# Performance work log

Measured on AMD Instinct MI355X. Metric: run time of the kernel, lower is better.

Reference implementation:

```python
import jax, jax.numpy as jnp
import numpy as np
from jax import lax


def _f(x, t, params):
    # Neural-ODE vector field: MLP acting on last dim (t unused, as allowed by arbitrary f)
    W1, b1, W2 = params
    return jnp.tanh(x @ W1 + b1) @ W2


def _euler_step(f, x, t, dt, params):
    return x + dt * f(x, t, params)


def _rk4_step(f, x, t, dt, params):
    # Replicates the source tableau EXACTLY, including its c-index offsets
    # (k2 uses t + c[0]*dt = t, k3 uses t + c[1]*dt, k4 uses t + c[2]*dt).
    c = (0.0, 0.5, 0.5, 1.0)
    k1 = f(x, t, params)
    k2 = f(x + dt * (0.5 * k1), t + c[0] * dt, params)
    k3 = f(x + dt * (0.5 * k2), t + c[1] * dt, params)
    k4 = f(x + dt * k3, t + c[2] * dt, params)
    return x + dt * (k1 / 6.0 + k2 / 3.0 + k3 / 3.0 + k4 / 6.0)


def _integrate(step, f, x, ts, params):
    # fixed_odeint with t = ts[k], dt = ts[k+1]-ts[k]; returns final state only
    dts = ts[1:] - ts[:-1]
    def body(xc, tdt):
        t, dt = tdt
        return step(f, xc, t, dt, params), None
    xf, _ = lax.scan(body, x, (ts[:-1], dts))
    return xf


def setup_inputs() -> dict:
    key = jax.random.key(0)
    k1, k2, k3 = jax.random.split(key, 3)
    n_sub, batch, d, h = 16, 256, 1024, 4096
    B = jax.random.normal(k1, (n_sub, batch, d), jnp.float32)
    t_span = jnp.arange(n_sub, dtype=jnp.float32)
    W1 = jax.random.normal(k2, (d, h), jnp.float32) * 0.02
    b1 = jnp.zeros((h,), jnp.float32)
    W2 = jax.random.normal(k3, (h, d), jnp.float32) * 0.02
    return {"B": B, "t_span": t_span, "W1": W1, "b1": b1, "W2": W2,
            "fine_steps": 8, "maxiter": 2}


def reference(B, t_span, W1, b1, W2, fine_steps, maxiter):
    params = (W1, b1, W2)
    n = B.shape[0]                       # n_subinterv
    dt = t_span[1] - t_span[0]
    sub_ts = jnp.linspace(0.0, dt, fine_steps)
    # Original: i = 0; while i <= maxiter: i += 1; body(i)  ->  i = 1..maxiter+1
    for i in range(1, maxiter + 2):
        # coarse (Euler) and fine (RK4) sweeps over all remaining nodes, vectorized
        B_coarse = _integrate(_euler_step, _f, B[i - 1:], sub_ts, params)  # [n-i+1,b,d]
        B_fine = _integrate(_rk4_step, _f, B[i - 1:], sub_ts, params)
        # sequential Parareal correction over nodes m = i..n-1
        def inner(B_in, cf):
            Bc, Bf = cf
            nxt = _integrate(_euler_step, _f, B_in, sub_ts, params) - Bc + Bf
            return nxt, nxt
        _, tail = lax.scan(inner, B[i - 1], (B_coarse[: n - i], B_fine[: n - i]))
        B = jnp.concatenate([B[:i], tail], axis=0)
    return B
```

## Files before the change

kernel.cpp:

```cpp
#include <hip/hip_runtime.h>
#include <cstdint>
#include <cstddef>


typedef __attribute__((ext_vector_type(4))) float f32x4;
typedef __attribute__((ext_vector_type(8))) short s16x8;
typedef __attribute__((ext_vector_type(4))) unsigned short u16x4;

#define DEV __device__ __forceinline__

DEV unsigned short f2bf(float x) {
  union { float f; uint32_t u; } v; v.f = x;
  uint32_t r = v.u + 0x7FFFu + ((v.u >> 16) & 1u);
  return (unsigned short)(r >> 16);
}
DEV float bf2f(unsigned short h) {
  union { uint32_t u; float f; } v; v.u = ((uint32_t)h) << 16; return v.f;
}
DEV void split2(float x, unsigned short &h, unsigned short &l) {
  h = f2bf(x);
  l = f2bf(x - bf2f(h));
}
DEV float fast_tanh(float z) {
  return 1.f - 2.f / (__expf(2.f * z) + 1.f);
}
DEV void gload16(const unsigned short* g, unsigned short* l) {
  __builtin_amdgcn_global_load_lds(
      (const __attribute__((address_space(1))) void*)g,
      (__attribute__((address_space(3))) void*)l, 16, 0, 0);
}

template<int EPI>
__global__ __launch_bounds__(256, 2) void gemm_k(
    const unsigned short* __restrict__ Ah, const unsigned short* __restrict__ Al,
    const unsigned short* __restrict__ Bh, const unsigned short* __restrict__ Bl,
    const float* __restrict__ bias,
    unsigned short* __restrict__ Oh, unsigned short* __restrict__ Ol,
    const float* __restrict__ Xin,
    float* __restrict__ ACCb,
    float* __restrict__ Xout,
    const float* __restrict__ tspan,
    float a1, float a2, int accAdd,
    int M, int N, int K, int KS)
{
  __shared__ unsigned short sA[2][128 * 64];
  __shared__ unsigned short sB[2][128 * 64];
  const int tid = threadIdx.x;
  const int w = tid >> 6, l = tid & 63;
  const int m0 = blockIdx.y * 128, n0 = blockIdx.x * 128;
  const int wm = (w >> 1) * 64, wn = (w & 1) * 64;

  f32x4 acc[4][4];
#pragma unroll
  for (int a = 0; a < 4; ++a)
#pragma unroll
    for (int b = 0; b < 4; ++b) acc[a][b] = (f32x4){0.f, 0.f, 0.f, 0.f};

  const int rsub = w * 8 + (l >> 3);
  const int ssrc = (l & 7) ^ (l >> 3);
  const int shalf = ssrc >> 2;
  const int schunk = ssrc & 3;
  const unsigned short* gA = (shalf ? Al : Ah) + (size_t)(m0 + rsub) * K + schunk * 8;
  const unsigned short* gB = (shalf ? Bl : Bh) + (size_t)(n0 + rsub) * K + schunk * 8;
  const size_t gstep = (size_t)32 * (size_t)K;
  const int db = w * 512;

  const int arow = (l & 15);
  const int slotH = ((l >> 4)) ^ (l & 7);
  const int slotL = (4 + (l >> 4)) ^ (l & 7);

  const int nk = KS >> 5;

  auto STAGE = [&](int buf, int kt) {
    const size_t ko = (size_t)kt * 32;
    unsigned short* da = &sA[buf][db];
    unsigned short* dbp = &sB[buf][db];
#pragma unroll
    for (int j = 0; j < 4; ++j) {
      gload16(gA + ko + (size_t)j * gstep, da + j * 2048);
      gload16(gB + ko + (size_t)j * gstep, dbp + j * 2048);
    }
  };

  STAGE(0, 0);
  __syncthreads();
  int cur = 0;

  for (int kt = 0; kt < nk; ++kt) {
    if (kt + 1 < nk) STAGE(cur ^ 1, kt + 1);
    const unsigned short* pa = &sA[cur][0];
    const unsigned short* pb = &sB[cur][0];
    s16x8 afh[4], afl[4], bfh[4], bfl[4];
#pragma unroll
    for (int mi = 0; mi < 4; ++mi) {
      const int rb = (wm + mi * 16 + arow) * 64;
      afh[mi] = *(const s16x8*)&pa[rb + slotH * 8];
      afl[mi] = *(const s16x8*)&pa[rb + slotL * 8];
    }
#pragma unroll
    for (int ni = 0; ni < 4; ++ni) {
      const int rb = (wn + ni * 16 + arow) * 64;
      bfh[ni] = *(const s16x8*)&pb[rb + slotH * 8];
      bfl[ni] = *(const s16x8*)&pb[rb + slotL * 8];
    }
#pragma unroll
    for (int mi = 0; mi < 4; ++mi)
#pragma unroll
      for (int ni = 0; ni < 4; ++ni) {
        acc[mi][ni] = __builtin_amdgcn_mfma_f32_16x16x32_bf16(afh[mi], bfh[ni], acc[mi][ni], 0, 0, 0);
        acc[mi][ni] = __builtin_amdgcn_mfma_f32_16x16x32_bf16(afh[mi], bfl[ni], acc[mi][ni], 0, 0, 0);
        acc[mi][ni] = __builtin_amdgcn_mfma_f32_16x16x32_bf16(afl[mi], bfh[ni], acc[mi][ni], 0, 0, 0);
      }
    __syncthreads();
    cur ^= 1;
  }

  const int colb = n0 + wn + (l & 15);
  const int rowb = m0 + wm + (l >> 4) * 4;
  const float sdt = (EPI >= 3) ? (tspan[1] - tspan[0]) * (1.0f / 7.0f) : 0.f;

  if (EPI == 1) {
#pragma unroll
    for (int mi = 0; mi < 4; ++mi)
#pragma unroll
      for (int ni = 0; ni < 4; ++ni) {
        const int col = colb + ni * 16;
        const float bc = bias[col];
#pragma unroll
        for (int j = 0; j < 4; ++j) {
          const size_t idx = (size_t)(rowb + mi * 16 + j) * N + col;
          const float v = fast_tanh(acc[mi][ni][j] + bc);
          unsigned short hh, ll; split2(v, hh, ll);
          Oh[idx] = hh; Ol[idx] = ll;
        }
      }
  } else if (EPI == 3) {
    const float c1 = a1 * sdt, c2 = a2 * sdt;
#pragma unroll
    for (int mi = 0; mi < 4; ++mi)
#pragma unroll
      for (int ni = 0; ni < 4; ++ni) {
        const int col = colb + ni * 16;
#pragma unroll
        for (int j = 0; j < 4; ++j) {
          const size_t idx = (size_t)(rowb + mi * 16 + j) * N + col;
          const float f = acc[mi][ni][j];
          const float x = Xin[idx];
          const float a = (accAdd ? ACCb[idx] : x) + c1 * f;
          ACCb[idx] = a;
          const float xt = x + c2 * f;
          unsigned short hh, ll; split2(xt, hh, ll);
          Oh[idx] = hh; Ol[idx] = ll;
        }
      }
  } else {
    const float coef = a1 + a2 * sdt;
#pragma unroll
    for (int mi = 0; mi < 4; ++mi)
#pragma unroll
      for (int ni = 0; ni < 4; ++ni) {
        const int col = colb + ni * 16;
#pragma unroll
        for (int j = 0; j < 4; ++j) {
          const size_t idx = (size_t)(rowb + mi * 16 + j) * N + col;
          const float v = Xin[idx] + coef * acc[mi][ni][j];
          Xout[idx] = v;
          unsigned short hh, ll; split2(v, hh, ll);
          Oh[idx] = hh; Ol[idx] = ll;
        }
      }
  }
}

template<int EPI>
__global__ __launch_bounds__(256, 2) void gemm64_k(
    const unsigned short* __restrict__ Ah, const unsigned short* __restrict__ Al,
    const unsigned short* __restrict__ Bh, const unsigned short* __restrict__ Bl,
    const float* __restrict__ bias,
    float* __restrict__ Part,
    unsigned short* __restrict__ Oh, unsigned short* __restrict__ Ol,
    int M, int N, int K, int KS)
{
  __shared__ unsigned short sA[2][64 * 64];
  __shared__ unsigned short sB[2][64 * 64];
  const int tid = threadIdx.x;
  const int w = tid >> 6, l = tid & 63;
  const int m0 = blockIdx.y * 64, n0 = blockIdx.x * 64;
  const size_t kbeg = (size_t)blockIdx.z * (size_t)KS;
  const int wm = (w >> 1) * 32, wn = (w & 1) * 32;

  f32x4 acc[2][2];
#pragma unroll
  for (int a = 0; a < 2; ++a)
#pragma unroll
    for (int b = 0; b < 2; ++b) acc[a][b] = (f32x4){0.f, 0.f, 0.f, 0.f};

  const int rsub = w * 8 + (l >> 3);
  const int ssrc = (l & 7) ^ (l >> 3);
  const int shalf = ssrc >> 2;
  const int schunk = ssrc & 3;
  const unsigned short* gA = (shalf ? Al : Ah) + (size_t)(m0 + rsub) * K + kbeg + schunk * 8;
  const unsigned short* gB = (shalf ? Bl : Bh) + (size_t)(n0 + rsub) * K + kbeg + schunk * 8;
  const size_t gstep = (size_t)32 * (size_t)K;
  const int db = w * 512;

  const int arow = (l & 15);
  const int slotH = ((l >> 4)) ^ (l & 7);
  const int slotL = (4 + (l >> 4)) ^ (l & 7);

  const int nk = KS >> 5;

  auto STAGE = [&](int buf, int kt) {
    const size_t ko = (size_t)kt * 32;
    unsigned short* da = &sA[buf][db];
    unsigned short* dbp = &sB[buf][db];
#pragma unroll
    for (int j = 0; j < 2; ++j) {
      gload16(gA + ko + (size_t)j * gstep, da + j * 2048);
      gload16(gB + ko + (size_t)j * gstep, dbp + j * 2048);
    }
  };

  STAGE(0, 0);
  __syncthreads();
  int cur = 0;

  for (int kt = 0; kt < nk; ++kt) {
    if (kt + 1 < nk) STAGE(cur ^ 1, kt + 1);
    const unsigned short* pa = &sA[cur][0];
    const unsigned short* pb = &sB[cur][0];
    s16x8 afh[2], afl[2], bfh[2], bfl[2];
#pragma unroll
    for (int mi = 0; mi < 2; ++mi) {
      const int rb = (wm + mi * 16 + arow) * 64;
      afh[mi] = *(const s16x8*)&pa[rb + slotH * 8];
      afl[mi] = *(const s16x8*)&pa[rb + slotL * 8];
    }
#pragma unroll
    for (int ni = 0; ni < 2; ++ni) {
      const int rb = (wn + ni * 16 + arow) * 64;
      bfh[ni] = *(const s16x8*)&pb[rb + slotH * 8];
      bfl[ni] = *(const s16x8*)&pb[rb + slotL * 8];
    }
#pragma unroll
    for (int mi = 0; mi < 2; ++mi)
#pragma unroll
      for (int ni = 0; ni < 2; ++ni) {
        acc[mi][ni] = __builtin_amdgcn_mfma_f32_16x16x32_bf16(afh[mi], bfh[ni], acc[mi][ni], 0, 0, 0);
        acc[mi][ni] = __builtin_amdgcn_mfma_f32_16x16x32_bf16(afh[mi], bfl[ni], acc[mi][ni], 0, 0, 0);
        acc[mi][ni] = __builtin_amdgcn_mfma_f32_16x16x32_bf16(afl[mi], bfh[ni], acc[mi][ni], 0, 0, 0);
      }
    __syncthreads();
    cur ^= 1;
  }

  const int colb = n0 + wn + (l & 15);
  const int rowb = m0 + wm + (l >> 4) * 4;

  if (EPI == 1) {
#pragma unroll
    for (int mi = 0; mi < 2; ++mi)
#pragma unroll
      for (int ni = 0; ni < 2; ++ni) {
        const int col = colb + ni * 16;
        const float bc = bias[col];
#pragma unroll
        for (int j = 0; j < 4; ++j) {
          const size_t idx = (size_t)(rowb + mi * 16 + j) * N + col;
          const float v = fast_tanh(acc[mi][ni][j] + bc);
          unsigned short hh, ll; split2(v, hh, ll);
          Oh[idx] = hh; Ol[idx] = ll;
        }
      }
  } else {
    float* dst = Part + (size_t)blockIdx.z * (size_t)M * N;
#pragma unroll
    for (int mi = 0; mi < 2; ++mi)
#pragma unroll
      for (int ni = 0; ni < 2; ++ni) {
        const int col = colb + ni * 16;
#pragma unroll
        for (int j = 0; j < 4; ++j)
          dst[(size_t)(rowb + mi * 16 + j) * N + col] = acc[mi][ni][j];
      }
  }
}

__global__ void reduce_axpy_k(const float* __restrict__ part, int S, int MN4,
    const float* __restrict__ tspan,
    float* __restrict__ Xf, unsigned short* __restrict__ Xh, unsigned short* __restrict__ Xl,
    const float* __restrict__ Dv, float* __restrict__ Bout, float* __restrict__ Eout)
{
  const int i = blockIdx.x * blockDim.x + threadIdx.x;
  if (i >= MN4) return;
  const float sdt = (tspan[1] - tspan[0]) * (1.0f / 7.0f);
  const size_t MN = (size_t)MN4 * 4;
  const size_t o = 4 * (size_t)i;
  f32x4 s = *(const f32x4*)(part + o);
  for (int z = 1; z < S; ++z) s += *(const f32x4*)(part + (size_t)z * MN + o);
  f32x4 e = *(const f32x4*)(Xf + o) + sdt * s;
  if (Eout) *(f32x4*)(Eout + o) = e;
  f32x4 v = e;
  if (Dv) v += *(const f32x4*)(Dv + o);
  *(f32x4*)(Xf + o) = v;
  u16x4 hh, ll;
#pragma unroll
  for (int j = 0; j < 4; ++j) { unsigned short h_, l_; split2(v[j], h_, l_); hh[j] = h_; ll[j] = l_; }
  *(u16x4*)(Xh + o) = hh;
  *(u16x4*)(Xl + o) = ll;
  if (Bout) *(f32x4*)(Bout + o) = v;
}

__global__ void axpy_split_k(
    float* __restrict__ dstF, unsigned short* __restrict__ dstH,
    unsigned short* __restrict__ dstL,
    const float* __restrict__ A, const float* __restrict__ Fv,
    float coef, int n4)
{
  for (int i = blockIdx.x * blockDim.x + threadIdx.x; i < n4;
       i += gridDim.x * blockDim.x) {
    const size_t o = 4 * (size_t)i;
    const f32x4 a = *(const f32x4*)(A + o);
    const f32x4 f = *(const f32x4*)(Fv + o);
    f32x4 v = a + coef * f;
    *(f32x4*)(dstF + o) = v;
    if (dstH) {
      u16x4 hh, ll;
#pragma unroll
      for (int j = 0; j < 4; ++j) { unsigned short h_, l_; split2(v[j], h_, l_); hh[j] = h_; ll[j] = l_; }
      *(u16x4*)(dstH + o) = hh;
      *(u16x4*)(dstL + o) = ll;
    }
  }
}

__global__ void transpose_split_k(const float* __restrict__ W,
                                  unsigned short* __restrict__ Th,
                                  unsigned short* __restrict__ Tl,
                                  int K, int N)
{
  __shared__ float t[32][33];
  const int tx = threadIdx.x & 31, ty = threadIdx.x >> 5;
  const int n0 = blockIdx.x * 32, k0 = blockIdx.y * 32;
#pragma unroll
  for (int r = 0; r < 4; ++r) {
    const int row = ty + r * 8;
    t[row][tx] = W[(size_t)(k0 + row) * N + n0 + tx];
  }
  __syncthreads();
#pragma unroll
  for (int r = 0; r < 4; ++r) {
    const int row = ty + r * 8;
    const float v = t[tx][row];
    unsigned short hh, ll; split2(v, hh, ll);
    const size_t idx = (size_t)(n0 + row) * K + k0 + tx;
    Th[idx] = hh; Tl[idx] = ll;
  }
}

extern "C" void kernel_launch(void* const* d_in, const int* in_sizes, int n_in,
                              void* d_out, int out_size, void* d_ws, size_t ws_size,
                              hipStream_t stream)
{
  const float* Bin   = (const float*)d_in[0];
  const float* tspan = (const float*)d_in[1];
  const float* W1    = (const float*)d_in[2];
  const float* b1    = (const float*)d_in[3];
  const float* W2    = (const float*)d_in[4];

  const int n = in_sizes[1];
  const int h = in_sizes[3];
  const int d = in_sizes[2] / h;
  const int batch = in_sizes[0] / (n * d);
  const int S = 7;
  const int MAXIT = 2;
  const size_t NB = (size_t)batch * d;

  float* Bw = (float*)d_out;

  uint8_t* wsb = (uint8_t*)d_ws;
  size_t off = 0;
  auto carve = [&](size_t bytes) -> void* {
    off = (off + 255) & ~(size_t)255;
    void* p = wsb + off; off += bytes; return p;
  };

  const size_t WH = (size_t)d * h;
  unsigned short* W1Th = (unsigned short*)carve(WH * 2);
  unsigned short* W1Tl = (unsigned short*)carve(WH * 2);
  unsigned short* W2Th = (unsigned short*)carve(WH * 2);
  unsigned short* W2Tl = (unsigned short*)carve(WH * 2);
  float* Dbuf = (float*)carve((size_t)(n - 1) * NB * 4);
  float* Eb   = (float*)carve((size_t)n * NB * 4);

  const int SPL2 = 4;
  float* Part = (float*)carve((size_t)SPL2 * NB * 4);

  const size_t per_node = NB * 20 + (size_t)batch * h * 4;
  int c;
  {
    size_t remb = ws_size > off + (1u << 20) ? ws_size - off - (1u << 20) : 0;
    c = (int)(remb / per_node);
    if (c < 1) c = 1;
    if (c > n - 1) c = n - 1;
  }
  const size_t CE = (size_t)c * NB;
  float*          Cst = (float*)carve(CE * 4);
  unsigned short* Csh = (unsigned short*)carve(CE * 2);
  unsigned short* Csl = (unsigned short*)carve(CE * 2);
  float*          Xf  = (float*)carve(CE * 4);
  unsigned short* Xh  = (unsigned short*)carve(CE * 2);
  unsigned short* Xl  = (unsigned short*)carve(CE * 2);
  float*          ACC = (float*)carve(CE * 4);
  unsigned short* Yh  = (unsigned short*)carve((size_t)c * batch * h * 2);
  unsigned short* Yl  = (unsigned short*)carve((size_t)c * batch * h * 2);
  unsigned short* XTh = Csh;
  unsigned short* XTl = Csl;

  auto ewg = [](size_t n4) -> int {
    size_t g = (n4 + 255) / 256;
    if (g > 2048) g = 2048; if (g < 1) g = 1;
    return (int)g;
  };
  auto axpy = [&](float* dF, unsigned short* dH, unsigned short* dL,
                  const float* A, const float* Fv, float coef, size_t ne) {
    const int n4 = (int)(ne / 4);
    axpy_split_k<<<ewg(n4), 256, 0, stream>>>(dF, dH, dL, A, Fv, coef, n4);
  };
  auto g1 = [&](const unsigned short* xh, const unsigned short* xl, int M) {
    gemm_k<1><<<dim3(h / 128, M / 128, 1), 256, 0, stream>>>(
        xh, xl, W1Th, W1Tl, b1, Yh, Yl,
        nullptr, nullptr, nullptr, tspan, 0.f, 0.f, 0, M, h, d, d);
  };
  auto g2rk = [&](int M, float a1, float a2, int add) {
    gemm_k<3><<<dim3(d / 128, M / 128, 1), 256, 0, stream>>>(
        Yh, Yl, W2Th, W2Tl, nullptr, XTh, XTl,
        Xf, ACC, nullptr, tspan, a1, a2, add, M, d, h, h);
  };
  auto g2ax = [&](int M, float* dF, unsigned short* dH, unsigned short* dL,
                  const float* Xin, float a1, float a2) {
    gemm_k<4><<<dim3(d / 128, M / 128, 1), 256, 0, stream>>>(
        Yh, Yl, W2Th, W2Tl, nullptr, dH, dL,
        Xin, nullptr, dF, tspan, a1, a2, 0, M, d, h, h);
  };

  hipMemcpyAsync(Bw, Bin, (size_t)n * NB * 4, hipMemcpyDeviceToDevice, stream);
  transpose_split_k<<<dim3(h / 32, d / 32), 256, 0, stream>>>(W1, W1Th, W1Tl, d, h);
  transpose_split_k<<<dim3(d / 32, h / 32), 256, 0, stream>>>(W2, W2Th, W2Tl, h, d);

  const int MN4d = (int)(NB / 4);

  for (int i = 1; i <= MAXIT + 1; ++i) {
    const int rem = n - i;

    for (int base = 0; base < rem; base += c) {
      const int cc = (rem - base) < c ? (rem - base) : c;
      const int M = cc * batch;
      const size_t ne = (size_t)M * d;
      const int j0 = i - 1 + base;
      const float* src = Bw + (size_t)j0 * NB;

      if (i == 1) {
        axpy(Cst, Csh, Csl, src, src, 0.f, ne);
        for (int s = 0; s < S; ++s) {
          g1(Csh, Csl, M);
          g2ax(M, Cst, Csh, Csl, Cst, 0.f, 1.f);
        }
      }
      axpy(Xf, Xh, Xl, src, src, 0.f, ne);
      for (int s = 0; s < S; ++s) {
        g1(Xh, Xl, M);   g2rk(M, 1.f / 6.f, 0.5f, 0);
        g1(XTh, XTl, M); g2rk(M, 1.f / 3.f, 0.5f, 1);
        g1(XTh, XTl, M); g2rk(M, 1.f / 3.f, 1.0f, 1);
        g1(XTh, XTl, M); g2ax(M, Xf, Xh, Xl, ACC, 0.f, 1.f / 6.f);
      }
      const float* Cref = (i == 1) ? Cst : (Eb + (size_t)j0 * NB);
      axpy(Dbuf + (size_t)base * NB, nullptr, nullptr, Xf, Cref, -1.f, ne);
    }

    const float* start = Bw + (size_t)(i - 1) * NB;
    axpy(Xf, Xh, Xl, start, start, 0.f, NB);
    for (int m = 0; m < rem; ++m) {
      for (int s = 0; s < S; ++s) {
        gemm64_k<1><<<dim3(h / 64, batch / 64, 1), 256, 0, stream>>>(
            Xh, Xl, W1Th, W1Tl, b1, nullptr, Yh, Yl, batch, h, d, d);
        gemm64_k<2><<<dim3(d / 64, batch / 64, SPL2), 256, 0, stream>>>(
            Yh, Yl, W2Th, W2Tl, nullptr, Part, nullptr, nullptr,
            batch, d, h, h / SPL2);
        const bool last = (s == S - 1);
        reduce_axpy_k<<<(MN4d + 255) / 256, 256, 0, stream>>>(
            Part, SPL2, MN4d, tspan, Xf, Xh, Xl,
            last ? Dbuf + (size_t)m * NB : nullptr,
            last ? Bw + (size_t)(i + m) * NB : nullptr,
            last ? Eb + (size_t)(i - 1 + m) * NB : nullptr);
      }
    }
  }
}
```

Before: 36.84 ms.

## Drop LDS double buffering and raise occupancy to three blocks per CU

Replaces the double-buffered LDS pipeline in the split-bf16 GEMM with a single buffer, loaded and then consumed between two barriers each K step. A fragments are loaded per row inside the MFMA loop, and launch bounds ask for three resident blocks per CU. The aim is to halve LDS use and cut registers so more waves hide latency. In exchange, global loads no longer overlap with MFMA work inside a block, so it depends on other blocks to cover that latency.

```diff
diff --git a/kernel.cpp b/kernel.cpp
--- a/kernel.cpp
+++ b/kernel.cpp
@@ -31,7 +31,7 @@
 }
 
 template<int EPI>
-__global__ __launch_bounds__(256, 2) void gemm_k(
+__global__ __launch_bounds__(256, 3) void gemm_k(
     const unsigned short* __restrict__ Ah, const unsigned short* __restrict__ Al,
     const unsigned short* __restrict__ Bh, const unsigned short* __restrict__ Bl,
     const float* __restrict__ bias,
@@ -43,8 +43,8 @@
     float a1, float a2, int accAdd,
     int M, int N, int K, int KS)
 {
-  __shared__ unsigned short sA[2][128 * 64];
-  __shared__ unsigned short sB[2][128 * 64];
+  __shared__ unsigned short sA[128 * 64];
+  __shared__ unsigned short sB[128 * 64];
   const int tid = threadIdx.x;
   const int w = tid >> 6, l = tid & 63;
   const int m0 = blockIdx.y * 128, n0 = blockIdx.x * 128;
@@ -71,48 +71,35 @@
 
   const int nk = KS >> 5;
 
-  auto STAGE = [&](int buf, int kt) {
+  for (int kt = 0; kt < nk; ++kt) {
     const size_t ko = (size_t)kt * 32;
-    unsigned short* da = &sA[buf][db];
-    unsigned short* dbp = &sB[buf][db];
 #pragma unroll
     for (int j = 0; j < 4; ++j) {
-      gload16(gA + ko + (size_t)j * gstep, da + j * 2048);
-      gload16(gB + ko + (size_t)j * gstep, dbp + j * 2048);
-    }
-  };
-
-  STAGE(0, 0);
-  __syncthreads();
-  int cur = 0;
-
-  for (int kt = 0; kt < nk; ++kt) {
-    if (kt + 1 < nk) STAGE(cur ^ 1, kt + 1);
-    const unsigned short* pa = &sA[cur][0];
-    const unsigned short* pb = &sB[cur][0];
-    s16x8 afh[4], afl[4], bfh[4], bfl[4];
+      gload16(gA + ko + (size_t)j * gstep, &sA[db + j * 2048]);
+      gload16(gB + ko + (size_t)j * gstep, &sB[db + j * 2048]);
+    }
+    __syncthreads();
+
+    s16x8 bfh[4], bfl[4];
+#pragma unroll
+    for (int ni = 0; ni < 4; ++ni) {
+      const int rb = (wn + ni * 16 + arow) * 64;
+      bfh[ni] = *(const s16x8*)&sB[rb + slotH * 8];
+      bfl[ni] = *(const s16x8*)&sB[rb + slotL * 8];
+    }
 #pragma unroll
     for (int mi = 0; mi < 4; ++mi) {
       const int rb = (wm + mi * 16 + arow) * 64;
-      afh[mi] = *(const s16x8*)&pa[rb + slotH * 8];
-      afl[mi] = *(const s16x8*)&pa[rb + slotL * 8];
-    }
-#pragma unroll
-    for (int ni = 0; ni < 4; ++ni) {
-      const int rb = (wn + ni * 16 + arow) * 64;
-      bfh[ni] = *(const s16x8*)&pb[rb + slotH * 8];
-      bfl[ni] = *(const s16x8*)&pb[rb + slotL * 8];
-    }
-#pragma unroll
-    for (int mi = 0; mi < 4; ++mi)
+      const s16x8 afh = *(const s16x8*)&sA[rb + slotH * 8];
+      const s16x8 afl = *(const s16x8*)&sA[rb + slotL * 8];
 #pragma unroll
       for (int ni = 0; ni < 4; ++ni) {
-        acc[mi][ni] = __builtin_amdgcn_mfma_f32_16x16x32_bf16(afh[mi], bfh[ni], acc[mi][ni], 0, 0, 0);
-        acc[mi][ni] = __builtin_amdgcn_mfma_f32_16x16x32_bf16(afh[mi], bfl[ni], acc[mi][ni], 0, 0, 0);
-        acc[mi][ni] = __builtin_amdgcn_mfma_f32_16x16x32_bf16(afl[mi], bfh[ni], acc[mi][ni], 0, 0, 0);
-      }
+        acc[mi][ni] = __builtin_amdgcn_mfma_f32_16x16x32_bf16(afh, bfh[ni], acc[mi][ni], 0, 0, 0);
+        acc[mi][ni] = __builtin_amdgcn_mfma_f32_16x16x32_bf16(afh, bfl[ni], acc[mi][ni], 0, 0, 0);
+        acc[mi][ni] = __builtin_amdgcn_mfma_f32_16x16x32_bf16(afl, bfh[ni], acc[mi][ni], 0, 0, 0);
+      }
+    }
     __syncthreads();
-    cur ^= 1;
   }
 
   const int colb = n0 + wn + (l & 15);
```

Result: no change. 37.42 ms (+1.6%).

## Add 256x256 tile GEMM for large first-layer GEMMs and XCD-aware block swizzle

Applied to the files above, without the earlier changes.

Adds a 512-thread kernel with 256x256 output tiles for the first MLP layer (tanh epilogue), used when M is at least 1024, to raise operand reuse per LDS load. It also remaps workgroup IDs in all GEMM kernels so consecutive logical tiles land on the same XCD, aiming for better L2 locality. The new kernel is single-buffered with two barriers per k-step, so global loads are not overlapped with MFMA work, and one block per CU lowers occupancy.

```diff
diff --git a/kernel.cpp b/kernel.cpp
--- a/kernel.cpp
+++ b/kernel.cpp
@@ -28,6 +28,19 @@
   __builtin_amdgcn_global_load_lds(
       (const __attribute__((address_space(1))) void*)g,
       (__attribute__((address_space(3))) void*)l, 16, 0, 0);
+}
+
+DEV void swz3(int &bx, int &by, int &bz) {
+  const int gx = gridDim.x, gy = gridDim.y, gz = gridDim.z;
+  const int nwg = gx * gy * gz;
+  const int lin = (bz * gy + by) * gx + bx;
+  const int q = nwg >> 3, r = nwg & 7;
+  const int x = lin & 7, j = lin >> 3;
+  const int logical = (x < r ? x * (q + 1) : r * (q + 1) + (x - r) * q) + j;
+  bx = logical % gx;
+  const int t = logical / gx;
+  by = t % gy;
+  bz = t / gy;
 }
 
 template<int EPI>
@@ -47,7 +60,9 @@
   __shared__ unsigned short sB[2][128 * 64];
   const int tid = threadIdx.x;
   const int w = tid >> 6, l = tid & 63;
-  const int m0 = blockIdx.y * 128, n0 = blockIdx.x * 128;
+  int bx = blockIdx.x, by = blockIdx.y, bz = blockIdx.z;
+  swz3(bx, by, bz);
+  const int m0 = by * 128, n0 = bx * 128;
   const int wm = (w >> 1) * 64, wn = (w & 1) * 64;
 
   f32x4 acc[4][4];
@@ -170,6 +185,93 @@
         }
       }
   }
+}
+
+__global__ __launch_bounds__(512, 1) void gemm256_k(
+    const unsigned short* __restrict__ Ah, const unsigned short* __restrict__ Al,
+    const unsigned short* __restrict__ Bh, const unsigned short* __restrict__ Bl,
+    const float* __restrict__ bias,
+    unsigned short* __restrict__ Oh, unsigned short* __restrict__ Ol,
+    int M, int N, int K)
+{
+  __shared__ unsigned short sA[256 * 64];
+  __shared__ unsigned short sB[256 * 64];
+  const int tid = threadIdx.x;
+  const int w = tid >> 6, l = tid & 63;
+  int bx = blockIdx.x, by = blockIdx.y, bz = blockIdx.z;
+  swz3(bx, by, bz);
+  const int m0 = by * 256, n0 = bx * 256;
+  const int wm = (w >> 2) * 128;
+  const int wn = (w & 3) * 64;
+
+  f32x4 acc[8][4];
+#pragma unroll
+  for (int a = 0; a < 8; ++a)
+#pragma unroll
+    for (int b = 0; b < 4; ++b) acc[a][b] = (f32x4){0.f, 0.f, 0.f, 0.f};
+
+  const int rsub = w * 8 + (l >> 3);
+  const int ssrc = (l & 7) ^ (l >> 3);
+  const int shalf = ssrc >> 2;
+  const int schunk = ssrc & 3;
+  const unsigned short* gA = (shalf ? Al : Ah) + (size_t)(m0 + rsub) * K + schunk * 8;
+  const unsigned short* gB = (shalf ? Bl : Bh) + (size_t)(n0 + rsub) * K + schunk * 8;
+  const size_t gstep = (size_t)64 * (size_t)K;
+  const int db = w * 512;
+
+  const int arow = (l & 15);
+  const int slotH = ((l >> 4)) ^ (l & 7);
+  const int slotL = (4 + (l >> 4)) ^ (l & 7);
+
+  const int nk = K >> 5;
+
+  for (int kt = 0; kt < nk; ++kt) {
+    const size_t ko = (size_t)kt * 32;
+#pragma unroll
+    for (int j = 0; j < 4; ++j) {
+      gload16(gA + ko + (size_t)j * gstep, &sA[db + j * 4096]);
+      gload16(gB + ko + (size_t)j * gstep, &sB[db + j * 4096]);
+    }
+    __syncthreads();
+
+    s16x8 bfh[4], bfl[4];
+#pragma unroll
+    for (int ni = 0; ni < 4; ++ni) {
+      const int rb = (wn + ni * 16 + arow) * 64;
+      bfh[ni] = *(const s16x8*)&sB[rb + slotH * 8];
+      bfl[ni] = *(const s16x8*)&sB[rb + slotL * 8];
+    }
+#pragma unroll
+    for (int mi = 0; mi < 8; ++mi) {
+      const int rb = (wm + mi * 16 + arow) * 64;
+      const s16x8 afh = *(const s16x8*)&sA[rb + slotH * 8];
+      const s16x8 afl = *(const s16x8*)&sA[rb + slotL * 8];
+#pragma unroll
+      for (int ni = 0; ni < 4; ++ni) {
+        acc[mi][ni] = __builtin_amdgcn_mfma_f32_16x16x32_bf16(afh, bfh[ni], acc[mi][ni], 0, 0, 0);
+        acc[mi][ni] = __builtin_amdgcn_mfma_f32_16x16x32_bf16(afh, bfl[ni], acc[mi][ni], 0, 0, 0);
+        acc[mi][ni] = __builtin_amdgcn_mfma_f32_16x16x32_bf16(afl, bfh[ni], acc[mi][ni], 0, 0, 0);
+      }
+    }
+    __syncthreads();
+  }
+
+  const int colb = n0 + wn + (l & 15);
+  const int rowb = m0 + wm + (l >> 4) * 4;
+#pragma unroll
+  for (int mi = 0; mi < 8; ++mi)
+#pragma unroll
+    for (int ni = 0; ni < 4; ++ni) {
+      const int col = colb + ni * 16;
+      const float bc = bias[col];
+#pragma unroll
+      for (int j = 0; j < 4; ++j) {
+        const size_t idx = (size_t)(rowb + mi * 16 + j) * N + col;
+        const float v = fast_tanh(acc[mi][ni][j] + bc);
+        unsigned short hh, ll; split2(v, hh, ll);
+        Oh[idx] = hh; Ol[idx] = ll;
+      }
+    }
 }
 
 template<int EPI>
@@ -185,8 +287,10 @@
   __shared__ unsigned short sB[2][64 * 64];
   const int tid = threadIdx.x;
   const int w = tid >> 6, l = tid & 63;
-  const int m0 = blockIdx.y * 64, n0 = blockIdx.x * 64;
-  const size_t kbeg = (size_t)blockIdx.z * (size_t)KS;
+  int bx = blockIdx.x, by = blockIdx.y, bz = blockIdx.z;
+  swz3(bx, by, bz);
+  const int m0 = by * 64, n0 = bx * 64;
+  const size_t kbeg = (size_t)bz * (size_t)KS;
   const int wm = (w >> 1) * 32, wn = (w & 1) * 32;
 
   f32x4 acc[2][2];
@@ -273,7 +377,7 @@
         }
       }
   } else {
-    float* dst = Part + (size_t)blockIdx.z * (size_t)M * N;
+    float* dst = Part + (size_t)bz * (size_t)M * N;
 #pragma unroll
     for (int mi = 0; mi < 2; ++mi)
 #pragma unroll
@@ -428,9 +532,14 @@
     axpy_split_k<<<ewg(n4), 256, 0, stream>>>(dF, dH, dL, A, Fv, coef, n4);
   };
   auto g1 = [&](const unsigned short* xh, const unsigned short* xl, int M) {
-    gemm_k<1><<<dim3(h / 128, M / 128, 1), 256, 0, stream>>>(
-        xh, xl, W1Th, W1Tl, b1, Yh, Yl,
-        nullptr, nullptr, nullptr, tspan, 0.f, 0.f, 0, M, h, d, d);
+    if (M >= 1024) {
+      gemm256_k<<<dim3(h / 256, M / 256, 1), 512, 0, stream>>>(
+          xh, xl, W1Th, W1Tl, b1, Yh, Yl, M, h, d);
+    } else {
+      gemm_k<1><<<dim3(h / 128, M / 128, 1), 256, 0, stream>>>(
+          xh, xl, W1Th, W1Tl, b1, Yh, Yl,
+          nullptr, nullptr, nullptr, tspan, 0.f, 0.f, 0, M, h, d, d);
+    }
   };
   auto g2rk = [&](int M, float a1, float a2, int add) {
     gemm_k<3><<<dim3(d / 128, M / 128, 1), 256, 0, stream>>>(
```

New measurement: 36.20 ms. No clear change (-1.7%).

## Switch GEMMs to 32x32x16 MFMA and add XCD-aware block swizzling

Applied to the files above, without the earlier changes.

Both GEMM kernels now use the 32x32x16 bf16 MFMA with 16-wide accumulators in place of the 16x16x32 variant. Each kernel loops over two k-halves per 32-wide LDS tile, and the epilogue index mapping is redone for the new output layout. Block indices are remapped so consecutive workgroups on the same XCD handle spatially clustered super-tiles, with the aim of better L2 reuse across the 8 XCDs. The larger MFMA needs fewer instructions and LDS reads per flop, but the remap and new fragment layout add integer overhead and risk indexing mistakes.

```diff
diff --git a/kernel.cpp b/kernel.cpp
--- a/kernel.cpp
+++ b/kernel.cpp
@@ -4,6 +4,7 @@
 
 
 typedef __attribute__((ext_vector_type(4))) float f32x4;
+typedef __attribute__((ext_vector_type(16))) float f32x16;
 typedef __attribute__((ext_vector_type(8))) short s16x8;
 typedef __attribute__((ext_vector_type(4))) unsigned short u16x4;
 
@@ -28,6 +29,26 @@
   __builtin_amdgcn_global_load_lds(
       (const __attribute__((address_space(1))) void*)g,
       (__attribute__((address_space(3))) void*)l, 16, 0, 0);
+}
+
+DEV void swz_st(int &bx, int &by, int &bz, int STX, int STY) {
+  const int gx = gridDim.x, gy = gridDim.y, gz = gridDim.z;
+  const int nwg = gx * gy * gz;
+  const int lin = (blockIdx.z * gy + blockIdx.y) * gx + blockIdx.x;
+  const int q = nwg >> 3, r = nwg & 7;
+  const int x = lin & 7, j = lin >> 3;
+  const int logical = (x < r ? x * (q + 1) : r * (q + 1) + (x - r) * q) + j;
+  const int plane = gx * gy;
+  bz = logical / plane;
+  const int p = logical % plane;
+  const int bps = STX * STY;
+  const int sgy = gy / STY;
+  const int stid = p / bps;
+  const int wid = p % bps;
+  const int stx = stid / sgy;
+  const int sty = stid % sgy;
+  bx = stx * STX + wid % STX;
+  by = sty * STY + wid / STX;
 }
 
 template<int EPI>
@@ -41,20 +62,24 @@
     float* __restrict__ Xout,
     const float* __restrict__ tspan,
     float a1, float a2, int accAdd,
-    int M, int N, int K, int KS)
+    int M, int N, int K, int KS, int STX, int STY)
 {
   __shared__ unsigned short sA[2][128 * 64];
   __shared__ unsigned short sB[2][128 * 64];
   const int tid = threadIdx.x;
   const int w = tid >> 6, l = tid & 63;
-  const int m0 = blockIdx.y * 128, n0 = blockIdx.x * 128;
+  int bx, by, bz;
+  swz_st(bx, by, bz, STX, STY);
+  const int m0 = by * 128, n0 = bx * 128;
   const int wm = (w >> 1) * 64, wn = (w & 1) * 64;
 
-  f32x4 acc[4][4];
-#pragma unroll
-  for (int a = 0; a < 4; ++a)
-#pragma unroll
-    for (int b = 0; b < 4; ++b) acc[a][b] = (f32x4){0.f, 0.f, 0.f, 0.f};
+  f32x16 acc[2][2];
+#pragma unroll
+  for (int a = 0; a < 2; ++a)
+#pragma unroll
+    for (int b = 0; b < 2; ++b)
+#pragma unroll
+      for (int r = 0; r < 16; ++r) acc[a][b][r] = 0.f;
 
   const int rsub = w * 8 + (l >> 3);
   const int ssrc = (l & 7) ^ (l >> 3);
@@ -65,9 +90,10 @@
   const size_t gstep = (size_t)32 * (size_t)K;
   const int db = w * 512;
 
-  const int arow = (l & 15);
-  const int slotH = ((l >> 4)) ^ (l & 7);
-  const int slotL = (4 + (l >> 4)) ^ (l & 7);
+  const int arow = l & 31;
+  const int kq = l >> 5;
+  const int sH[2] = { (kq) ^ (l & 7), (2 + kq) ^ (l & 7) };
+  const int sL[2] = { (4 + kq) ^ (l & 7), (6 + kq) ^ (l & 7) };
 
   const int nk = KS >> 5;
 
@@ -90,46 +116,49 @@
     if (kt + 1 < nk) STAGE(cur ^ 1, kt + 1);
     const unsigned short* pa = &sA[cur][0];
     const unsigned short* pb = &sB[cur][0];
-    s16x8 afh[4], afl[4], bfh[4], bfl[4];
-#pragma unroll
-    for (int mi = 0; mi < 4; ++mi) {
-      const int rb = (wm + mi * 16 + arow) * 64;
-      afh[mi] = *(const s16x8*)&pa[rb + slotH * 8];
-      afl[mi] = *(const s16x8*)&pa[rb + slotL * 8];
-    }
-#pragma unroll
-    for (int ni = 0; ni < 4; ++ni) {
-      const int rb = (wn + ni * 16 + arow) * 64;
-      bfh[ni] = *(const s16x8*)&pb[rb + slotH * 8];
-      bfl[ni] = *(const s16x8*)&pb[rb + slotL * 8];
-    }
-#pragma unroll
-    for (int mi = 0; mi < 4; ++mi)
-#pragma unroll
-      for (int ni = 0; ni < 4; ++ni) {
-        acc[mi][ni] = __builtin_amdgcn_mfma_f32_16x16x32_bf16(afh[mi], bfh[ni], acc[mi][ni], 0, 0, 0);
-        acc[mi][ni] = __builtin_amdgcn_mfma_f32_16x16x32_bf16(afh[mi], bfl[ni], acc[mi][ni], 0, 0, 0);
-        acc[mi][ni] = __builtin_amdgcn_mfma_f32_16x16x32_bf16(afl[mi], bfh[ni], acc[mi][ni], 0, 0, 0);
-      }
+#pragma unroll
+    for (int kh = 0; kh < 2; ++kh) {
+      const int sh = sH[kh], sl = sL[kh];
+      s16x8 bfh[2], bfl[2];
+#pragma unroll
+      for (int ni = 0; ni < 2; ++ni) {
+        const int rb = (wn + ni * 32 + arow) * 64;
+        bfh[ni] = *(const s16x8*)&pb[rb + sh * 8];
+        bfl[ni] = *(const s16x8*)&pb[rb + sl * 8];
+      }
+#pragma unroll
+      for (int mi = 0; mi < 2; ++mi) {
+        const int ra = (wm + mi * 32 + arow) * 64;
+        const s16x8 afh = *(const s16x8*)&pa[ra + sh * 8];
+        const s16x8 afl = *(const s16x8*)&pa[ra + sl * 8];
+#pragma unroll
+        for (int ni = 0; ni < 2; ++ni) {
+          acc[mi][ni] = __builtin_amdgcn_mfma_f32_32x32x16_bf16(afh, bfh[ni], acc[mi][ni], 0, 0, 0);
+          acc[mi][ni] = __builtin_amdgcn_mfma_f32_32x32x16_bf16(afh, bfl[ni], acc[mi][ni], 0, 0, 0);
+          acc[mi][ni] = __builtin_amdgcn_mfma_f32_32x32x16_bf16(afl, bfh[ni], acc[mi][ni], 0, 0, 0);
+        }
+      }
+    }
     __syncthreads();
     cur ^= 1;
   }
 
-  const int colb = n0 + wn + (l & 15);
-  const int rowb = m0 + wm + (l >> 4) * 4;
+  const int colb = n0 + wn + (l & 31);
+  const int rowb = m0 + wm + 4 * (l >> 5);
   const float sdt = (EPI >= 3) ? (tspan[1] - tspan[0]) * (1.0f / 7.0f) : 0.f;
 
   if (EPI == 1) {
 #pragma unroll
-    for (int mi = 0; mi < 4; ++mi)
-#pragma unroll
-      for (int ni = 0; ni < 4; ++ni) {
-        const int col = colb + ni * 16;
+    for (int mi = 0; mi < 2; ++mi)
+#pragma unroll
+      for (int ni = 0; ni < 2; ++ni) {
+        const int col = colb + ni * 32;
         const float bc = bias[col];
 #pragma unroll
-        for (int j = 0; j < 4; ++j) {
-          const size_t idx = (size_t)(rowb + mi * 16 + j) * N + col;
-          const float v = fast_tanh(acc[mi][ni][j] + bc);
+        for (int r = 0; r < 16; ++r) {
+          const int row = rowb + mi * 32 + (r & 3) + 8 * (r >> 2);
+          const size_t idx = (size_t)row * N + col;
+          const float v = fast_tanh(acc[mi][ni][r] + bc);
           unsigned short hh, ll; split2(v, hh, ll);
           Oh[idx] = hh; Ol[idx] = ll;
         }
@@ -137,14 +166,15 @@
   } else if (EPI == 3) {
     const float c1 = a1 * sdt, c2 = a2 * sdt;
 #pragma unroll
-    for (int mi = 0; mi < 4; ++mi)
-#pragma unroll
-      for (int ni = 0; ni < 4; ++ni) {
-        const int col = colb + ni * 16;
-#pragma unroll
-        for (int j = 0; j < 4; ++j) {
-          const size_t idx = (size_t)(rowb + mi * 16 + j) * N + col;
-          const float f = acc[mi][ni][j];
+    for (int mi = 0; mi < 2; ++mi)
+#pragma unroll
+      for (int ni = 0; ni < 2; ++ni) {
+        const int col = colb + ni * 32;
+#pragma unroll
+        for (int r = 0; r < 16; ++r) {
+          const int row = rowb + mi * 32 + (r & 3) + 8 * (r >> 2);
+          const size_t idx = (size_t)row * N + col;
+          const float f = acc[mi][ni][r];
           const float x = Xin[idx];
           const float a = (accAdd ? ACCb[idx] : x) + c1 * f;
           ACCb[idx] = a;
@@ -156,14 +186,15 @@
   } else {
     const float coef = a1 + a2 * sdt;
 #pragma unroll
-    for (int mi = 0; mi < 4; ++mi)
-#pragma unroll
-      for (int ni = 0; ni < 4; ++ni) {
-        const int col = colb + ni * 16;
-#pragma unroll
-        for (int j = 0; j < 4; ++j) {
-          const size_t idx = (size_t)(rowb + mi * 16 + j) * N + col;
-          const float v = Xin[idx] + coef * acc[mi][ni][j];
+    for (int mi = 0; mi < 2; ++mi)
+#pragma unroll
+      for (int ni = 0; ni < 2; ++ni) {
+        const int col = colb + ni * 32;
+#pragma unroll
+        for (int r = 0; r < 16; ++r) {
+          const int row = rowb + mi * 32 + (r & 3) + 8 * (r >> 2);
+          const size_t idx = (size_t)row * N + col;
+          const float v = Xin[idx] + coef * acc[mi][ni][r];
           Xout[idx] = v;
           unsigned short hh, ll; split2(v, hh, ll);
           Oh[idx] = hh; Ol[idx] = ll;
@@ -179,21 +210,21 @@
     const float* __restrict__ bias,
     float* __restrict__ Part,
     unsigned short* __restrict__ Oh, unsigned short* __restrict__ Ol,
-    int M, int N, int K, int KS)
+    int M, int N, int K, int KS, int STX, int STY)
 {
   __shared__ unsigned short sA[2][64 * 64];
   __shared__ unsigned short sB[2][64 * 64];
   const int tid = threadIdx.x;
   const int w = tid >> 6, l = tid & 63;
-  const int m0 = blockIdx.y * 64, n0 = blockIdx.x * 64;
-  const size_t kbeg = (size_t)blockIdx.z * (size_t)KS;
+  int bx, by, bz;
+  swz_st(bx, by, bz, STX, STY);
+  const int m0 = by * 64, n0 = bx * 64;
+  const size_t kbeg = (size_t)bz * (size_t)KS;
   const int wm = (w >> 1) * 32, wn = (w & 1) * 32;
 
-  f32x4 acc[2][2];
-#pragma unroll
-  for (int a = 0; a < 2; ++a)
-#pragma unroll
-    for (int b = 0; b < 2; ++b) acc[a][b] = (f32x4){0.f, 0.f, 0.f, 0.f};
+  f32x16 acc;
+#pragma unroll
+  for (int r = 0; r < 16; ++r) acc[r] = 0.f;
 
   const int rsub = w * 8 + (l >> 3);
   const int ssrc = (l & 7) ^ (l >> 3);
@@ -204,9 +235,10 @@
   const size_t gstep = (size_t)32 * (size_t)K;
   const int db = w * 512;
 
-  const int arow = (l & 15);
-  const int slotH = ((l >> 4)) ^ (l & 7);
-  const int slotL = (4 + (l >> 4)) ^ (l & 7);
+  const int arow = l & 31;
+  const int kq = l >> 5;
+  const int sH[2] = { (kq) ^ (l & 7), (2 + kq) ^ (l & 7) };
+  const int sL[2] = { (4 + kq) ^ (l & 7), (6 + kq) ^ (l & 7) };
 
   const int nk = KS >> 5;
 
@@ -229,60 +261,43 @@
     if (kt + 1 < nk) STAGE(cur ^ 1, kt + 1);
     const unsigned short* pa = &sA[cur][0];
     const unsigned short* pb = &sB[cur][0];
-    s16x8 afh[2], afl[2], bfh[2], bfl[2];
-#pragma unroll
-    for (int mi = 0; mi < 2; ++mi) {
-      const int rb = (wm + mi * 16 + arow) * 64;
-      afh[mi] = *(const s16x8*)&pa[rb + slotH * 8];
-      afl[mi] = *(const s16x8*)&pa[rb + slotL * 8];
-    }
-#pragma unroll
-    for (int ni = 0; ni < 2; ++ni) {
-      const int rb = (wn + ni * 16 + arow) * 64;
-      bfh[ni] = *(const s16x8*)&pb[rb + slotH * 8];
-      bfl[ni] = *(const s16x8*)&pb[rb + slotL * 8];
-    }
-#pragma unroll
-    for (int mi = 0; mi < 2; ++mi)
-#pragma unroll
-      for (int ni = 0; ni < 2; ++ni) {
-        acc[mi][ni] = __builtin_amdgcn_mfma_f32_16x16x32_bf16(afh[mi], bfh[ni], acc[mi][ni], 0, 0, 0);
-        acc[mi][ni] = __builtin_amdgcn_mfma_f32_16x16x32_bf16(afh[mi], bfl[ni], acc[mi][ni], 0, 0, 0);
-        acc[mi][ni] = __builtin_amdgcn_mfma_f32_16x16x32_bf16(afl[mi], bfh[ni], acc[mi][ni], 0, 0, 0);
-      }
+#pragma unroll
+    for (int kh = 0; kh < 2; ++kh) {
+      const int sh = sH[kh], sl = sL[kh];
+      const int rb = (wn + arow) * 64;
+      const int ra = (wm + arow) * 64;
+      const s16x8 bfh = *(const s16x8*)&pb[rb + sh * 8];
+      const s16x8 bfl = *(const s16x8*)&pb[rb + sl * 8];
+      const s16x8 afh = *(const s16x8*)&pa[ra + sh * 8];
+      const s16x8 afl = *(const s16x8*)&pa[ra + sl * 8];
+      acc = __builtin_amdgcn_mfma_f32_32x32x16_bf16(afh, bfh, acc, 0, 0, 0);
+      acc = __builtin_amdgcn_mfma_f32_32x32x16_bf16(afh, bfl, acc, 0, 0, 0);
+      acc = __builtin_amdgcn_mfma_f32_32x32x16_bf16(afl, bfh, acc, 0, 0, 0);
+    }
     __syncthreads();
     cur ^= 1;
   }
 
-  const int colb = n0 + wn + (l & 15);
-  const int rowb = m0 + wm + (l >> 4) * 4;
+  const int col = n0 + wn + (l & 31);
+  const int rowb = m0 + wm + 4 * (l >> 5);
 
   if (EPI == 1) {
-#pragma unroll
-    for (int mi = 0; mi < 2; ++mi)
-#pragma unroll
-      for (int ni = 0; ni < 2; ++ni) {
-        const int col = colb + ni * 16;
-        const float bc = bias[col];
-#pragma unroll
-        for (int j = 0; j < 4; ++j) {
-          const size_t idx = (size_t)(rowb + mi * 16 + j) * N + col;
-          const float v = fast_tanh(acc[mi][ni][j] + bc);
-          unsigned short hh, ll; split2(v, hh, ll);
-          Oh[idx] = hh; Ol[idx] = ll;
-        }
-      }
+    const float bc = bias[col];
+#pragma unroll
+    for (int r = 0; r < 16; ++r) {
+      const int row = rowb + (r & 3) + 8 * (r >> 2);
+      const size_t idx = (size_t)row * N + col;
+      const float v = fast_tanh(acc[r] + bc);
+      unsigned short hh, ll; split2(v, hh, ll);
+      Oh[idx] = hh; Ol[idx] = ll;
+    }
   } else {
-    float* dst = Part + (size_t)blockIdx.z * (size_t)M * N;
-#pragma unroll
-    for (int mi = 0; mi < 2; ++mi)
-#pragma unroll
-      for (int ni = 0; ni < 2; ++ni) {
-        const int col = colb + ni * 16;
-#pragma unroll
-        for (int j = 0; j < 4; ++j)
-          dst[(size_t)(rowb + mi * 16 + j) * N + col] = acc[mi][ni][j];
-      }
+    float* dst = Part + (size_t)bz * (size_t)M * N;
+#pragma unroll
+    for (int r = 0; r < 16; ++r) {
+      const int row = rowb + (r & 3) + 8 * (r >> 2);
+      dst[(size_t)row * N + col] = acc[r];
+    }
   }
 }
 
@@ -417,6 +432,11 @@
   unsigned short* XTh = Csh;
   unsigned short* XTl = Csl;
 
+  auto pickst = [](int g, int want) {
+    int s = want;
+    while (s > 1 && (g % s)) s >>= 1;
+    return s;
+  };
   auto ewg = [](size_t n4) -> int {
     size_t g = (n4 + 255) / 256;
     if (g > 2048) g = 2048; if (g < 1) g = 1;
@@ -428,20 +448,26 @@
     axpy_split_k<<<ewg(n4), 256, 0, stream>>>(dF, dH, dL, A, Fv, coef, n4);
   };
   auto g1 = [&](const unsigned short* xh, const unsigned short* xl, int M) {
-    gemm_k<1><<<dim3(h / 128, M / 128, 1), 256, 0, stream>>>(
+    const int gy = M / 128;
+    gemm_k<1><<<dim3(h / 128, gy, 1), 256, 0, stream>>>(
         xh, xl, W1Th, W1Tl, b1, Yh, Yl,
-        nullptr, nullptr, nullptr, tspan, 0.f, 0.f, 0, M, h, d, d);
+        nullptr, nullptr, nullptr, tspan, 0.f, 0.f, 0, M, h, d, d,
+        pickst(h / 128, 8), pickst(gy, 4));
   };
   auto g2rk = [&](int M, float a1, float a2, int add) {
-    gemm_k<3><<<dim3(d / 128, M / 128, 1), 256, 0, stream>>>(
+    const int gy = M / 128;
+    gemm_k<3><<<dim3(d / 128, gy, 1), 256, 0, stream>>>(
         Yh, Yl, W2Th, W2Tl, nullptr, XTh, XTl,
-        Xf, ACC, nullptr, tspan, a1, a2, add, M, d, h, h);
+        Xf, ACC, nullptr, tspan, a1, a2, add, M, d, h, h,
+        pickst(d / 128, 4), pickst(gy, 4));
   };
   auto g2ax = [&](int M, float* dF, unsigned short* dH, unsigned short* dL,
                   const float* Xin, float a1, float a2) {
-    gemm_k<4><<<dim3(d / 128, M / 128, 1), 256, 0, stream>>>(
+    const int gy = M / 128;
+    gemm_k<4><<<dim3(d / 128, gy, 1), 256, 0, stream>>>(
         Yh, Yl, W2Th, W2Tl, nullptr, dH, dL,
-        Xin, nullptr, dF, tspan, a1, a2, 0, M, d, h, h);
+        Xin, nullptr, dF, tspan, a1, a2, 0, M, d, h, h,
+        pickst(d / 128, 4), pickst(gy, 4));
   };
 
   hipMemcpyAsync(Bw, Bin, (size_t)n * NB * 4, hipMemcpyDeviceToDevice, stream);
@@ -483,10 +509,12 @@
     for (int m = 0; m < rem; ++m) {
       for (int s = 0; s < S; ++s) {
         gemm64_k<1><<<dim3(h / 64, batch / 64, 1), 256, 0, stream>>>(
-            Xh, Xl, W1Th, W1Tl, b1, nullptr, Yh, Yl, batch, h, d, d);
+            Xh, Xl, W1Th, W1Tl, b1, nullptr, Yh, Yl, batch, h, d, d,
+            pickst(h / 64, 8), pickst(batch / 64, 4));
         gemm64_k<2><<<dim3(d / 64, batch / 64, SPL2), 256, 0, stream>>>(
             Yh, Yl, W2Th, W2Tl, nullptr, Part, nullptr, nullptr,
-            batch, d, h, h / SPL2);
+            batch, d, h, h / SPL2,
+            pickst(d / 64, 8), pickst(batch / 64, 4));
         const bool last = (s == S - 1);
         reduce_axpy_k<<<(MN4d + 255) / 256, 256, 0, stream>>>(
             Part, SPL2, MN4d, tspan, Xf, Xh, Xl,
```

After: 35.49 ms. 1.04x faster.
